# Kernel tuning notes

Hardware: AMD Instinct MI355X
Metric: run time of the kernel (lower is better)

## Reference

```python
import jax, jax.numpy as jnp
import numpy as np

EPS = 1e-5

def _batchnorm(x, gamma, beta):
    # BatchNorm1d in training mode: stats over the point (N) dimension, biased var
    mean = x.mean(axis=0)
    var = ((x - mean) ** 2).mean(axis=0)
    return (x - mean) * jax.lax.rsqrt(var + EPS) * gamma + beta

def setup_inputs() -> dict:
    key = jax.random.key(0)
    ks = jax.random.split(key, 6)
    N, C_in, K, B = 262144, 3, 64, 16
    return {
        "feats": jax.random.normal(ks[0], (N, C_in), dtype=jnp.float32),
        "batch_idx": jax.random.randint(ks[1], (N,), 0, B, dtype=jnp.int32),
        "W1": jax.random.normal(ks[2], (128, C_in), dtype=jnp.float32) * 0.1,
        "gamma1": jnp.ones((128,), jnp.float32),
        "beta1": jnp.zeros((128,), jnp.float32),
        "W2": jax.random.normal(ks[3], (64, 256), dtype=jnp.float32) * 0.05,
        "gamma2": jnp.ones((64,), jnp.float32),
        "beta2": jnp.zeros((64,), jnp.float32),
        "W3": jax.random.normal(ks[4], (K, 64), dtype=jnp.float32) * 0.1,
        "b3": jnp.zeros((K,), jnp.float32),
        "num_batches": B,
    }

def reference(feats, batch_idx, W1, gamma1, beta1, W2, gamma2, beta2, W3, b3, num_batches):
    # conv1 (1x1 conv == linear, no bias) + bn1
    x = _batchnorm(feats @ W1.T, gamma1, beta1)          # [N,128]
    # per-batch global max pooling, broadcast back to points
    seg_max = jax.ops.segment_max(x, batch_idx, num_segments=num_batches)  # [B,128]
    x = jnp.concatenate([x, seg_max[batch_idx]], axis=1)  # [N,256]
    # conv2 + bn2 + relu
    x = jax.nn.relu(_batchnorm(x @ W2.T, gamma2, beta2))  # [N,64]
    # conv3 (with bias)
    return x @ W3.T + b3                                   # [N,k]
```

## Files before the change

kernel.cpp:

```cpp
#include <hip/hip_runtime.h>
#include <hip/hip_bf16.h>

#define EPS 1e-5f
#define NPTS 262144
#define NB 16
#define ACBLK 1024

typedef __attribute__((ext_vector_type(8))) short bf16x8;
typedef __attribute__((ext_vector_type(4))) float f32x4;

#define WS_E    0
#define WS_T    192
#define WS_W3   1216
#define WS_MAXF 3264
#define WS_PMOM 5312
#define WS_SCRM 6480
#define WS_SMAX 81232

__device__ inline float decodeu(unsigned u){
  unsigned bits = (u & 0x80000000u) ? (u ^ 0x80000000u) : ~u;
  return __uint_as_float(bits);
}
__device__ inline unsigned f2bf(float f){
  unsigned u = __float_as_uint(f);
  return (u + 0x7FFFu + ((u>>16)&1u)) >> 16;
}
__device__ inline unsigned pack2bf(float lo, float hi){
  return (f2bf(hi)<<16) | (f2bf(lo) & 0xFFFFu);
}
__device__ inline unsigned ordu(float v){
  unsigned bits = __float_as_uint(v);
  return bits ^ (unsigned)(((int)bits>>31) | (int)0x80000000);
}

__global__ __launch_bounds__(256) void kAC(const float* __restrict__ feats,
                                           const int* __restrict__ bidx,
                                           const float* __restrict__ W1,
                                           const float* __restrict__ g1,
                                           float* __restrict__ wsf) {
  __shared__ unsigned lmax[NB*128];
  __shared__ __align__(16) float4 sfeat[256];
  __shared__ float hist[NB*4];
  __shared__ float red[4*9];
  int tid = threadIdx.x;
  for (int i=tid;i<NB*128;i+=256) lmax[i]=0u;
  if (tid < NB*4) hist[tid]=0.f;
  __syncthreads();
  int p = blockIdx.x*256 + tid;
  float f0=feats[3*p], f1=feats[3*p+1], f2=feats[3*p+2];
  int b = bidx[p];
  sfeat[tid] = make_float4(f0,f1,f2,__int_as_float(b));
  atomicAdd(&hist[b*4+0],f0);
  atomicAdd(&hist[b*4+1],f1);
  atomicAdd(&hist[b*4+2],f2);
  atomicAdd(&hist[b*4+3],1.0f);
  int lane = tid&63, wv = tid>>6;
  { float acc[9]={f0,f1,f2,f0*f0,f0*f1,f0*f2,f1*f1,f1*f2,f2*f2};
    #pragma unroll
    for (int k=0;k<9;k++){
      float v=acc[k];
      v+=__shfl_down(v,32); v+=__shfl_down(v,16); v+=__shfl_down(v,8);
      v+=__shfl_down(v,4);  v+=__shfl_down(v,2);  v+=__shfl_down(v,1);
      if (lane==0) red[wv*9+k]=v;
    }
  }
  __syncthreads();
  int c0 = lane, c1 = lane+64;
  float sg0 = (g1[c0]>=0.f)?1.f:-1.f;
  float sg1 = (g1[c1]>=0.f)?1.f:-1.f;
  float w00=W1[3*c0]*sg0, w01=W1[3*c0+1]*sg0, w02=W1[3*c0+2]*sg0;
  float w10=W1[3*c1]*sg1, w11=W1[3*c1+1]*sg1, w12=W1[3*c1+2]*sg1;
  const float4* sp = &sfeat[wv*64];
  float m0[16], m1[16];
  #pragma unroll
  for (int q=0;q<16;q++){ m0[q] = -__builtin_inff(); m1[q] = -__builtin_inff(); }
  #pragma unroll 8
  for (int k=0;k<64;k++){
    float4 f = sp[k];
    float v0 = fmaf(f.z,w02,fmaf(f.y,w01,f.x*w00));
    float v1 = fmaf(f.z,w12,fmaf(f.y,w11,f.x*w10));
    int sbb = __builtin_amdgcn_readfirstlane(__float_as_int(f.w));
    switch (sbb){
      case 0:  m0[0]=fmaxf(m0[0],v0);  m1[0]=fmaxf(m1[0],v1);  break;
      case 1:  m0[1]=fmaxf(m0[1],v0);  m1[1]=fmaxf(m1[1],v1);  break;
      case 2:  m0[2]=fmaxf(m0[2],v0);  m1[2]=fmaxf(m1[2],v1);  break;
      case 3:  m0[3]=fmaxf(m0[3],v0);  m1[3]=fmaxf(m1[3],v1);  break;
      case 4:  m0[4]=fmaxf(m0[4],v0);  m1[4]=fmaxf(m1[4],v1);  break;
      case 5:  m0[5]=fmaxf(m0[5],v0);  m1[5]=fmaxf(m1[5],v1);  break;
      case 6:  m0[6]=fmaxf(m0[6],v0);  m1[6]=fmaxf(m1[6],v1);  break;
      case 7:  m0[7]=fmaxf(m0[7],v0);  m1[7]=fmaxf(m1[7],v1);  break;
      case 8:  m0[8]=fmaxf(m0[8],v0);  m1[8]=fmaxf(m1[8],v1);  break;
      case 9:  m0[9]=fmaxf(m0[9],v0);  m1[9]=fmaxf(m1[9],v1);  break;
      case 10: m0[10]=fmaxf(m0[10],v0); m1[10]=fmaxf(m1[10],v1); break;
      case 11: m0[11]=fmaxf(m0[11],v0); m1[11]=fmaxf(m1[11],v1); break;
      case 12: m0[12]=fmaxf(m0[12],v0); m1[12]=fmaxf(m1[12],v1); break;
      case 13: m0[13]=fmaxf(m0[13],v0); m1[13]=fmaxf(m1[13],v1); break;
      case 14: m0[14]=fmaxf(m0[14],v0); m1[14]=fmaxf(m1[14],v1); break;
      default: m0[15]=fmaxf(m0[15],v0); m1[15]=fmaxf(m1[15],v1); break;
    }
  }
  #pragma unroll
  for (int q=0;q<16;q++){
    if (m0[q] > -__builtin_inff()) atomicMax(&lmax[q*128+c0], ordu(m0[q]));
    if (m1[q] > -__builtin_inff()) atomicMax(&lmax[q*128+c1], ordu(m1[q]));
  }
  __syncthreads();
  float* scrM = wsf + WS_SCRM + blockIdx.x*73;
  if (tid<9) scrM[tid]=red[tid]+red[9+tid]+red[18+tid]+red[27+tid];
  if (tid>=64 && tid<128) scrM[9+tid-64]=hist[tid-64];
  unsigned* spo = (unsigned*)wsf + WS_SMAX + (size_t)blockIdx.x*2048;
  for (int i=tid;i<2048;i+=256) spo[i]=lmax[i];
}

__global__ __launch_bounds__(256) void kMx(const float* __restrict__ W3,
                                           float* __restrict__ wsf){
  __shared__ unsigned red[8][32];
  __shared__ float mred[2][73];
  int tid = threadIdx.x, blk = blockIdx.x;
  int g = tid >> 5;
  int e = blk*32 + (tid & 31);
  const unsigned* smax = (const unsigned*)wsf + WS_SMAX;
  unsigned m = 0;
  #pragma unroll 4
  for (int k=g*128; k<g*128+128; k++){
    unsigned t = smax[(size_t)k*2048 + e];
    m = t>m ? t : m;
  }
  red[g][tid&31] = m;
  if (blk < 16 && tid < 146){
    int h = (tid >= 73) ? 1 : 0, mm = tid - 73*h;
    float s = 0; const float* sm0 = wsf + WS_SCRM;
    int k0 = blk*64 + h*32;
    #pragma unroll 4
    for (int k=k0; k<k0+32; k++) s += sm0[k*73 + mm];
    mred[h][mm] = s;
  }
  if (blk >= 16 && blk < 20){
    int q = (blk-16)*256 + tid;
    float4 v = ((const float4*)W3)[q];
    unsigned* w3u = (unsigned*)wsf + WS_W3;
    w3u[2*q]   = pack2bf(v.x, v.y);
    w3u[2*q+1] = pack2bf(v.z, v.w);
  }
  __syncthreads();
  if (tid < 32){
    unsigned u = red[0][tid];
    #pragma unroll
    for (int q=1;q<8;q++){ unsigned t=red[q][tid]; u = t>u?t:u; }
    ((unsigned*)wsf)[WS_MAXF + blk*32 + tid] = u;
  }
  if (blk < 16 && tid < 73)
    wsf[WS_PMOM + blk*73 + tid] = mred[0][tid] + mred[1][tid];
}

__global__ __launch_bounds__(128) void kB2(const float* __restrict__ W1,
    const float* __restrict__ g1, const float* __restrict__ b1,
    const float* __restrict__ W2, const float* __restrict__ g2,
    const float* __restrict__ b2, float* __restrict__ wsf){
  __shared__ float smom[80];
  __shared__ float dred[2][20];
  int tid = threadIdx.x, c = blockIdx.x;
  int lane = tid & 63, wv = tid >> 6;
  if (tid < 73){
    float s = 0; const float* pm = wsf + WS_PMOM;
    #pragma unroll
    for (int g=0; g<16; g++) s += pm[g*73 + tid];
    smom[tid] = s;
  }
  int j = tid;
  float w2f = W2[c*256 + j];
  float w2b = W2[c*256 + 128 + j];
  float w10 = W1[3*j], w11 = W1[3*j+1], w12 = W1[3*j+2];
  float g1j = g1[j], b1j = b1[j];
  unsigned um[16];
  { const unsigned* mf = (const unsigned*)wsf + WS_MAXF;
    #pragma unroll
    for (int b=0;b<16;b++) um[b] = mf[b*128 + j];
  }
  __syncthreads();
  const float invN = 1.0f/NPTS;
  float mean = (w10*smom[0]+w11*smom[1]+w12*smom[2])*invN;
  float ex2 = (w10*w10*smom[3]+w11*w11*smom[6]+w12*w12*smom[8]
             + 2.f*(w10*w11*smom[4]+w10*w12*smom[5]+w11*w12*smom[7]))*invN;
  float var = ex2 - mean*mean;
  float sc = g1j*rsqrtf(var+EPS);
  float sh = b1j - mean*sc;
  float asc = fabsf(sc);
  float p[20];
  p[0] = w2f*(sc*w10); p[1] = w2f*(sc*w11); p[2] = w2f*(sc*w12); p[3] = w2f*sh;
  #pragma unroll
  for (int b=0;b<16;b++) p[4+b] = w2b * fmaf(asc, decodeu(um[b]), sh);
  #pragma unroll
  for (int k=0;k<20;k++){
    float v = p[k];
    v+=__shfl_down(v,32); v+=__shfl_down(v,16); v+=__shfl_down(v,8);
    v+=__shfl_down(v,4);  v+=__shfl_down(v,2);  v+=__shfl_down(v,1);
    if (lane==0) dred[wv][k] = v;
  }
  __syncthreads();
  if (tid == 0){
    float fin[20];
    #pragma unroll
    for (int k=0;k<20;k++) fin[k] = dred[0][k] + dred[1][k];
    float e0=fin[0], e1=fin[1], e2=fin[2], gc=fin[3];
    float sumY = e0*smom[0]+e1*smom[1]+e2*smom[2];
    float sumYY = e0*e0*smom[3]+e1*e1*smom[6]+e2*e2*smom[8]
               + 2.f*(e0*e1*smom[4]+e0*e2*smom[5]+e1*e2*smom[7]);
    float hbs[16];
    #pragma unroll
    for (int b=0;b<16;b++){
      float nb = smom[9+b*4+3];
      float hb = gc + fin[4+b];
      hbs[b] = hb;
      float eS1b = e0*smom[9+b*4]+e1*smom[9+b*4+1]+e2*smom[9+b*4+2];
      sumY += nb*hb;
      sumYY += 2.f*hb*eS1b + nb*hb*hb;
    }
    float mean2 = sumY*invN;
    float var2 = sumYY*invN - mean2*mean2;
    float s2 = g2[c]*rsqrtf(var2+EPS);
    float t2 = b2[c] - mean2*s2;
    wsf[WS_E + c]      = e0*s2;
    wsf[WS_E + 64 + c] = e1*s2;
    wsf[WS_E + 128 + c]= e2*s2;
    #pragma unroll
    for (int b=0;b<16;b++) wsf[WS_T + b*64 + c] = hbs[b]*s2 + t2;
  }
}

__global__ __launch_bounds__(256, 4) void kF(const float* __restrict__ feats,
                                             const int* __restrict__ bidx,
                                             const float* __restrict__ wsf,
                                             const float* __restrict__ b3,
                                             float* __restrict__ out) {
  __shared__ __align__(16) unsigned char SB[36992];
  unsigned* zbuf = (unsigned*)SB;
  float* Tl = (float*)(SB + 32768);
  float* fbuf = (float*)SB;
  int tid = threadIdx.x;
  for (int i=tid;i<NB*64;i+=256) Tl[(i>>6)*66 + (i&63)] = wsf[WS_T + i];
  int lane = tid & 63, wv = tid >> 6;
  int col = lane & 15, kgrp = lane >> 4;
  const ushort* w3b = (const ushort*)((const unsigned*)wsf + WS_W3);
  bf16x8 bfr[4][2];
  #pragma unroll
  for (int n=0;n<4;n++)
    #pragma unroll
    for (int kk=0;kk<2;kk++)
      bfr[n][kk] = *(const bf16x8*)(w3b + (n*16+col)*64 + kk*32 + kgrp*8);
  float bias[4];
  #pragma unroll
  for (int n=0;n<4;n++) bias[n] = b3[n*16+col];
  __syncthreads();
  const float* Eg = wsf + WS_E;
  int p0 = (blockIdx.x*4 + wv)*64;
  int p = p0 + lane;
  float f0 = feats[3*p], f1 = feats[3*p+1], f2 = feats[3*p+2];
  int b = bidx[p];
  const float* tb = &Tl[b*66];
  unsigned rowbase = (unsigned)(wv*64+lane)*32;
  unsigned sw = (lane&7)<<2;
  #pragma unroll
  for (int j=0;j<8;j++){
    unsigned w[4];
    #pragma unroll
    for (int q=0;q<4;q++){
      int c = j*8 + q*2;
      float2 tp = *(const float2*)(tb + c);
      float y0 = fmaf(Eg[c],  f0, fmaf(Eg[64+c],  f1, fmaf(Eg[128+c],  f2, tp.x)));
      float y1 = fmaf(Eg[c+1],f0, fmaf(Eg[64+c+1],f1, fmaf(Eg[128+c+1],f2, tp.y)));
      w[q] = pack2bf(fmaxf(y0,0.f), fmaxf(y1,0.f));
    }
    uint4 ch; ch.x=w[0]; ch.y=w[1]; ch.z=w[2]; ch.w=w[3];
    *(uint4*)&zbuf[rowbase + (((unsigned)(j*4)) ^ sw)] = ch;
  }
  __syncthreads();
  bf16x8 af[4][2];
  #pragma unroll
  for (int m=0;m<4;m++){
    int row = m*16 + col;
    unsigned rb = (unsigned)(wv*64+row)*32;
    unsigned sw2 = (unsigned)(row&7)<<2;
    #pragma unroll
    for (int kk=0;kk<2;kk++){
      unsigned off = ((unsigned)(kk*16 + kgrp*4)) ^ sw2;
      af[m][kk] = *(const bf16x8*)&zbuf[rb + off];
    }
  }
  __syncthreads();
  #pragma unroll
  for (int half=0; half<2; half++){
    f32x4 acc[2][4];
    #pragma unroll
    for (int mi=0;mi<2;mi++)
      #pragma unroll
      for (int n=0;n<4;n++)
        acc[mi][n] = (f32x4){0.f,0.f,0.f,0.f};
    #pragma unroll
    for (int kk=0;kk<2;kk++)
      #pragma unroll
      for (int mi=0;mi<2;mi++)
        #pragma unroll
        for (int n=0;n<4;n++)
          acc[mi][n] = __builtin_amdgcn_mfma_f32_16x16x32_bf16(af[half*2+mi][kk], bfr[n][kk], acc[mi][n], 0,0,0);
    #pragma unroll
    for (int mi=0;mi<2;mi++){
      #pragma unroll
      for (int n=0;n<4;n++){
        #pragma unroll
        for (int r=0;r<4;r++)
          fbuf[wv*2176 + (mi*16 + kgrp*4 + r)*68 + n*16 + col] = acc[mi][n][r] + bias[n];
      }
    }
    __syncthreads();
    #pragma unroll
    for (int it=0; it<8; it++){
      int idx = it*256 + tid;
      int gr = idx >> 4;
      int c4 = (idx & 15) * 4;
      float4 v = *(const float4*)&fbuf[(gr>>5)*2176 + (gr&31)*68 + c4];
      int orow = blockIdx.x*256 + (gr>>5)*64 + half*32 + (gr&31);
      *(float4*)&out[(size_t)orow*64 + c4] = v;
    }
    __syncthreads();
  }
}

extern "C" void kernel_launch(void* const* d_in, const int* in_sizes, int n_in,
                              void* d_out, int out_size, void* d_ws, size_t ws_size,
                              hipStream_t stream) {
  const float* feats = (const float*)d_in[0];
  const int*   bidx  = (const int*)d_in[1];
  const float* W1 = (const float*)d_in[2];
  const float* g1 = (const float*)d_in[3];
  const float* b1 = (const float*)d_in[4];
  const float* W2 = (const float*)d_in[5];
  const float* g2 = (const float*)d_in[6];
  const float* b2 = (const float*)d_in[7];
  const float* W3 = (const float*)d_in[8];
  const float* b3 = (const float*)d_in[9];
  float* wsf = (float*)d_ws;
  float* out = (float*)d_out;
  kAC<<<ACBLK, 256, 0, stream>>>(feats, bidx, W1, g1, wsf);
  kMx<<<64, 256, 0, stream>>>(W3, wsf);
  kB2<<<64, 128, 0, stream>>>(W1, g1, b1, W2, g2, b2, wsf);
  kF<<<ACBLK, 256, 0, stream>>>(feats, bidx, wsf, b3, out);
}
```

Before: 62.55 us.

## Bucket points by batch in kAC, widen kMx reduction, use nontemporal stores

kAC now counting-sorts each block's points by batch index in shared memory. Each wave can then keep one running max per channel and flush it with an atomic only when the batch changes, replacing 32 per-batch register accumulators and a wave-uniform switch. kMx moves to 512 threads with half the rows per thread group and uses nontemporal loads. Stores of the partial maxima and of the final output become nontemporal. The sort adds two barriers and a serial prefix sum in a single thread, and the nontemporal hints change cache behaviour for data that the next kernel reads back.

After: 62.67 us. Within noise of the previous version (+0.2%).

```diff
diff --git a/kernel.cpp b/kernel.cpp
--- a/kernel.cpp
+++ b/kernel.cpp
@@ -42,19 +42,21 @@
   __shared__ __align__(16) float4 sfeat[256];
   __shared__ float hist[NB*4];
   __shared__ float red[4*9];
+  __shared__ unsigned cnt[NB], base[NB];
   int tid = threadIdx.x;
+  int lane = tid&63, wv = tid>>6;
   for (int i=tid;i<NB*128;i+=256) lmax[i]=0u;
   if (tid < NB*4) hist[tid]=0.f;
+  if (tid < NB) cnt[tid]=0u;
   __syncthreads();
   int p = blockIdx.x*256 + tid;
   float f0=feats[3*p], f1=feats[3*p+1], f2=feats[3*p+2];
   int b = bidx[p];
-  sfeat[tid] = make_float4(f0,f1,f2,__int_as_float(b));
   atomicAdd(&hist[b*4+0],f0);
   atomicAdd(&hist[b*4+1],f1);
   atomicAdd(&hist[b*4+2],f2);
   atomicAdd(&hist[b*4+3],1.0f);
-  int lane = tid&63, wv = tid>>6;
+  unsigned pos = atomicAdd(&cnt[b], 1u);
   { float acc[9]={f0,f1,f2,f0*f0,f0*f1,f0*f2,f1*f1,f1*f2,f2*f2};
     #pragma unroll
     for (int k=0;k<9;k++){
@@ -64,6 +66,14 @@
       if (lane==0) red[wv*9+k]=v;
     }
   }
+  __syncthreads();
+  if (tid==0){
+    unsigned s=0;
+    #pragma unroll
+    for (int q=0;q<NB;q++){ base[q]=s; s+=cnt[q]; }
+  }
+  __syncthreads();
+  sfeat[base[b]+pos] = make_float4(f0,f1,f2,__int_as_float(b));
   __syncthreads();
   int c0 = lane, c1 = lane+64;
   float sg0 = (g1[c0]>=0.f)?1.f:-1.f;
@@ -71,59 +81,45 @@
   float w00=W1[3*c0]*sg0, w01=W1[3*c0+1]*sg0, w02=W1[3*c0+2]*sg0;
   float w10=W1[3*c1]*sg1, w11=W1[3*c1+1]*sg1, w12=W1[3*c1+2]*sg1;
   const float4* sp = &sfeat[wv*64];
-  float m0[16], m1[16];
-  #pragma unroll
-  for (int q=0;q<16;q++){ m0[q] = -__builtin_inff(); m1[q] = -__builtin_inff(); }
+  int bcur = -1; float mm0=0.f, mm1=0.f;
   #pragma unroll 8
   for (int k=0;k<64;k++){
     float4 f = sp[k];
     float v0 = fmaf(f.z,w02,fmaf(f.y,w01,f.x*w00));
     float v1 = fmaf(f.z,w12,fmaf(f.y,w11,f.x*w10));
-    int sbb = __builtin_amdgcn_readfirstlane(__float_as_int(f.w));
-    switch (sbb){
-      case 0:  m0[0]=fmaxf(m0[0],v0);  m1[0]=fmaxf(m1[0],v1);  break;
-      case 1:  m0[1]=fmaxf(m0[1],v0);  m1[1]=fmaxf(m1[1],v1);  break;
-      case 2:  m0[2]=fmaxf(m0[2],v0);  m1[2]=fmaxf(m1[2],v1);  break;
-      case 3:  m0[3]=fmaxf(m0[3],v0);  m1[3]=fmaxf(m1[3],v1);  break;
-      case 4:  m0[4]=fmaxf(m0[4],v0);  m1[4]=fmaxf(m1[4],v1);  break;
-      case 5:  m0[5]=fmaxf(m0[5],v0);  m1[5]=fmaxf(m1[5],v1);  break;
-      case 6:  m0[6]=fmaxf(m0[6],v0);  m1[6]=fmaxf(m1[6],v1);  break;
-      case 7:  m0[7]=fmaxf(m0[7],v0);  m1[7]=fmaxf(m1[7],v1);  break;
-      case 8:  m0[8]=fmaxf(m0[8],v0);  m1[8]=fmaxf(m1[8],v1);  break;
-      case 9:  m0[9]=fmaxf(m0[9],v0);  m1[9]=fmaxf(m1[9],v1);  break;
-      case 10: m0[10]=fmaxf(m0[10],v0); m1[10]=fmaxf(m1[10],v1); break;
-      case 11: m0[11]=fmaxf(m0[11],v0); m1[11]=fmaxf(m1[11],v1); break;
-      case 12: m0[12]=fmaxf(m0[12],v0); m1[12]=fmaxf(m1[12],v1); break;
-      case 13: m0[13]=fmaxf(m0[13],v0); m1[13]=fmaxf(m1[13],v1); break;
-      case 14: m0[14]=fmaxf(m0[14],v0); m1[14]=fmaxf(m1[14],v1); break;
-      default: m0[15]=fmaxf(m0[15],v0); m1[15]=fmaxf(m1[15],v1); break;
-    }
-  }
-  #pragma unroll
-  for (int q=0;q<16;q++){
-    if (m0[q] > -__builtin_inff()) atomicMax(&lmax[q*128+c0], ordu(m0[q]));
-    if (m1[q] > -__builtin_inff()) atomicMax(&lmax[q*128+c1], ordu(m1[q]));
-  }
+    int b2 = __builtin_amdgcn_readfirstlane(__float_as_int(f.w));
+    if (b2 != bcur){
+      if (bcur >= 0){
+        atomicMax(&lmax[bcur*128+c0], ordu(mm0));
+        atomicMax(&lmax[bcur*128+c1], ordu(mm1));
+      }
+      bcur = b2; mm0 = v0; mm1 = v1;
+    } else {
+      mm0 = fmaxf(mm0,v0); mm1 = fmaxf(mm1,v1);
+    }
+  }
+  atomicMax(&lmax[bcur*128+c0], ordu(mm0));
+  atomicMax(&lmax[bcur*128+c1], ordu(mm1));
   __syncthreads();
   float* scrM = wsf + WS_SCRM + blockIdx.x*73;
   if (tid<9) scrM[tid]=red[tid]+red[9+tid]+red[18+tid]+red[27+tid];
   if (tid>=64 && tid<128) scrM[9+tid-64]=hist[tid-64];
   unsigned* spo = (unsigned*)wsf + WS_SMAX + (size_t)blockIdx.x*2048;
-  for (int i=tid;i<2048;i+=256) spo[i]=lmax[i];
-}
-
-__global__ __launch_bounds__(256) void kMx(const float* __restrict__ W3,
+  for (int i=tid;i<2048;i+=256) __builtin_nontemporal_store(lmax[i], &spo[i]);
+}
+
+__global__ __launch_bounds__(512) void kMx(const float* __restrict__ W3,
                                            float* __restrict__ wsf){
-  __shared__ unsigned red[8][32];
+  __shared__ unsigned red[16][32];
   __shared__ float mred[2][73];
   int tid = threadIdx.x, blk = blockIdx.x;
   int g = tid >> 5;
   int e = blk*32 + (tid & 31);
   const unsigned* smax = (const unsigned*)wsf + WS_SMAX;
   unsigned m = 0;
-  #pragma unroll 4
-  for (int k=g*128; k<g*128+128; k++){
-    unsigned t = smax[(size_t)k*2048 + e];
+  #pragma unroll 8
+  for (int k=g*64; k<g*64+64; k++){
+    unsigned t = __builtin_nontemporal_load(&smax[(size_t)k*2048 + e]);
     m = t>m ? t : m;
   }
   red[g][tid&31] = m;
@@ -135,8 +131,8 @@
     for (int k=k0; k<k0+32; k++) s += sm0[k*73 + mm];
     mred[h][mm] = s;
   }
-  if (blk >= 16 && blk < 20){
-    int q = (blk-16)*256 + tid;
+  if (blk >= 16 && blk < 18){
+    int q = (blk-16)*512 + tid;
     float4 v = ((const float4*)W3)[q];
     unsigned* w3u = (unsigned*)wsf + WS_W3;
     w3u[2*q]   = pack2bf(v.x, v.y);
@@ -146,7 +142,7 @@
   if (tid < 32){
     unsigned u = red[0][tid];
     #pragma unroll
-    for (int q=1;q<8;q++){ unsigned t=red[q][tid]; u = t>u?t:u; }
+    for (int q=1;q<16;q++){ unsigned t=red[q][tid]; u = t>u?t:u; }
     ((unsigned*)wsf)[WS_MAXF + blk*32 + tid] = u;
   }
   if (blk < 16 && tid < 73)
@@ -318,9 +314,9 @@
       int idx = it*256 + tid;
       int gr = idx >> 4;
       int c4 = (idx & 15) * 4;
-      float4 v = *(const float4*)&fbuf[(gr>>5)*2176 + (gr&31)*68 + c4];
+      f32x4 v = *(const f32x4*)&fbuf[(gr>>5)*2176 + (gr&31)*68 + c4];
       int orow = blockIdx.x*256 + (gr>>5)*64 + half*32 + (gr&31);
-      *(float4*)&out[(size_t)orow*64 + c4] = v;
+      __builtin_nontemporal_store(v, (f32x4*)&out[(size_t)orow*64 + c4]);
     }
     __syncthreads();
   }
@@ -342,7 +338,7 @@
   float* wsf = (float*)d_ws;
   float* out = (float*)d_out;
   kAC<<<ACBLK, 256, 0, stream>>>(feats, bidx, W1, g1, wsf);
-  kMx<<<64, 256, 0, stream>>>(W3, wsf);
+  kMx<<<64, 512, 0, stream>>>(W3, wsf);
   kB2<<<64, 128, 0, stream>>>(W1, g1, b1, W2, g2, b2, wsf);
   kF<<<ACBLK, 256, 0, stream>>>(feats, bidx, wsf, b3, out);
 }
```
